# Performance work log

Hardware: AMD Instinct MI355X
Metric: run time of the kernel (lower is better)

## Reference

```python
import jax, jax.numpy as jnp
import numpy as np

N_SENT = 20  # sentence_number


def setup_inputs() -> dict:
    key = jax.random.key(0)
    k1, k2, k3, k4, k5 = jax.random.split(key, 5)
    B, S, D, U = 2048, 800, 100, 50
    inputs = jax.random.normal(k1, (B, S + 1, D), dtype=jnp.float32)
    # keras 'random_normal' initializer default stddev = 0.05
    vw = 0.05 * jax.random.normal(k2, (U, 1), dtype=jnp.float32)
    wh = 0.05 * jax.random.normal(k3, (U, D), dtype=jnp.float32)
    wu = 0.05 * jax.random.normal(k4, (U, D), dtype=jnp.float32)
    bw = 0.05 * jax.random.normal(k5, (U, 1), dtype=jnp.float32)
    return {"inputs": inputs, "vw": vw, "wh": wh, "wu": wu, "bw": bw}


def reference(inputs, vw, wh, wu, bw):
    # inputs: [B, S+1, D]; last row of each item is the user vector
    sent = inputs[:, :-1, :]          # [B, S, D]
    uvec = inputs[:, -1, :]           # [B, D]
    B, S, D = sent.shape
    sec = S // N_SENT
    h = sent.reshape(B, N_SENT, sec, D)               # sections of sentences
    # wu @ user_vec + bw  -> per-batch additive bias  [B, units]
    wub = uvec @ wu.T + bw[:, 0]
    # tanh(h @ wh.T + wub)                              [B, n, s, units]
    t = jnp.tanh(jnp.einsum('bnsd,ud->bnsu', h, wh) + wub[:, None, None, :])
    e = jnp.einsum('bnsu,u->bns', t, vw[:, 0])          # attention logits
    alpha = jax.nn.softmax(e, axis=-1)                  # softmax over section
    out = jnp.einsum('bns,bnsd->bnd', alpha, h)         # weighted pooling
    return out  # [B, N_SENT, D]
```

## Files before the change

kernel.cpp:

```cpp
#include <hip/hip_runtime.h>
#include <hip/hip_bf16.h>
#include <stdint.h>

#define NB    2048
#define NSENT 20
#define SEC   40
#define DD    100
#define UU    50
#define SP1   801
#define STRIDE 136

typedef short bf16x8 __attribute__((ext_vector_type(8)));
typedef float f32x4 __attribute__((ext_vector_type(4)));

__device__ __forceinline__ unsigned f2bf(float f) {
  unsigned u = __float_as_uint(f);
  return (u + 0x7fffu + ((u >> 16) & 1u)) >> 16;
}

__global__ __launch_bounds__(256, 4) void doc_kernel(
    const float* __restrict__ inputs, const float* __restrict__ vw,
    const float* __restrict__ wh, const float* __restrict__ wu,
    const float* __restrict__ bw, float* __restrict__ out) {
  __shared__ __align__(16) unsigned short hs[2][48 * STRIDE];
  __shared__ __align__(16) float epart[3 * 16 * 4];

  const int tid  = threadIdx.x;
  const int w    = tid >> 6, lane = tid & 63;
  const int col  = lane & 15, grp = lane >> 4;
  const int b    = blockIdx.x;

  const float4* base4 = (const float4*)(inputs + (size_t)b * SP1 * DD);

  float4 stA[4], stB[4];
  #pragma unroll
  for (int j = 0; j < 4; ++j) stA[j] = base4[j * 256 + tid];
  #pragma unroll
  for (int j = 0; j < 4; ++j) stB[j] = base4[1000 + j * 256 + tid];

  {
    uint4 z; z.x = z.y = z.z = z.w = 0u;
    uint4* p = (uint4*)&hs[0][0];
    #pragma unroll 1
    for (int i = tid; i < 2 * 48 * STRIDE / 8; i += 256) p[i] = z;
  }

  int cvta[4];
  #pragma unroll
  for (int j = 0; j < 4; ++j) {
    int idx = j * 256 + tid;
    int row = idx / 25, c4 = idx - row * 25;
    cvta[j] = row * 272 + c4 * 8;
  }

  bf16x8 afrag[4];
  {
    int u = w * 16 + col;
    #pragma unroll
    for (int kt = 0; kt < 4; ++kt) {
      bf16x8 f;
      #pragma unroll
      for (int j = 0; j < 8; ++j) {
        int k = kt * 32 + grp * 8 + j;
        float v = (u < UU && k < DD) ? wh[u * DD + k] : 0.f;
        f[j] = (short)f2bf(v);
      }
      afrag[kt] = f;
    }
  }

  float wubacc;
  {
    int ur = lane < UU ? lane : UU - 1;
    const float4* uv4 = (const float4*)(inputs + ((size_t)b * SP1 + SP1 - 1) * DD);
    const float4* wr4 = (const float4*)(wu + ur * DD);
    float a0 = bw[ur];
    #pragma unroll 5
    for (int q = 0; q < 25; ++q) {
      float4 uq = uv4[q], wq = wr4[q];
      a0 = fmaf(uq.x, wq.x, a0); a0 = fmaf(uq.y, wq.y, a0);
      a0 = fmaf(uq.z, wq.z, a0); a0 = fmaf(uq.w, wq.w, a0);
    }
    wubacc = a0;
  }
  float vwr[4], wubr[4];
  #pragma unroll
  for (int r = 0; r < 4; ++r) {
    int u = w * 16 + grp * 4 + r;
    float wv = __shfl(wubacc, u & 63);
    bool val = (u < UU);
    vwr[r]  = val ? vw[u] : 0.f;
    wubr[r] = val ? wv : 0.f;
  }

  __syncthreads();

  float* outb = out + (size_t)b * NSENT * DD;

#define TILE_BODY(stg, t)                                                      \
  {                                                                            \
    unsigned char* hc = (unsigned char*)&hs[(t) & 1][0];                       \
                     \
    _Pragma("unroll")                                                          \
    for (int j = 0; j < 4; ++j) {                                              \
      unsigned o0, o1;                                                         \
      asm("v_cvt_pk_bf16_f32 %0, %1, %2" : "=v"(o0) : "v"(stg[j].x), "v"(stg[j].y)); \
      asm("v_cvt_pk_bf16_f32 %0, %1, %2" : "=v"(o1) : "v"(stg[j].z), "v"(stg[j].w)); \
      uint2 wv; wv.x = o0; wv.y = o1;                                          \
      *(uint2*)(hc + cvta[j]) = wv;                                            \
    }                                                                          \
      \
    if ((t) + 2 < NSENT) {                                                     \
      const float4* nb4 = base4 + (size_t)((t) + 2) * 1000;                    \
      _Pragma("unroll")                                                        \
      for (int j = 0; j < 4; ++j) stg[j] = nb4[j * 256 + tid];                 \
    }                                                                          \
    __builtin_amdgcn_sched_barrier(0);                                         \
    __syncthreads();                                                   \
                                   \
    f32x4 acc[3];                                                              \
    _Pragma("unroll")                                                          \
    for (int st = 0; st < 3; ++st) { f32x4 z = {0.f,0.f,0.f,0.f}; acc[st] = z; } \
    _Pragma("unroll")                                                          \
    for (int kt = 0; kt < 4; ++kt) {                                           \
      _Pragma("unroll")                                                        \
      for (int st = 0; st < 3; ++st) {                                         \
        bf16x8 hf = *(const bf16x8*)(hc + (st * 16 + col) * 272 + kt * 64 + grp * 16); \
        acc[st] = __builtin_amdgcn_mfma_f32_16x16x32_bf16(afrag[kt], hf, acc[st], 0, 0, 0); \
      }                                                                        \
    }                                                                          \
                                \
    _Pragma("unroll")                                                          \
    for (int st = 0; st < 3; ++st) {                                           \
      float s = 0.f;                                                           \
      _Pragma("unroll")                                                        \
      for (int r = 0; r < 4; ++r) {                                            \
        float x = acc[st][r] + wubr[r];                                        \
        float E = __expf(2.f * x);                                             \
        float tt = 1.f - 2.f * __builtin_amdgcn_rcpf(E + 1.f);                 \
        s = fmaf(tt, vwr[r], s);                                               \
      }                                                                        \
      s += __shfl_xor(s, 16);                                                  \
      s += __shfl_xor(s, 32);                                                  \
      if (grp == 0) epart[st * 64 + col * 4 + w] = s;                          \
    }                                                                          \
    __syncthreads();                                                   \
             \
    int sl = lane < SEC ? lane : 0;                                            \
    f32x4 q = *(const f32x4*)&epart[(sl >> 4) * 64 + (sl & 15) * 4];           \
    float e = (q[0] + q[1]) + (q[2] + q[3]);                                   \
    float p = (lane < SEC) ? __expf(e) : 0.f;                                  \
    float sum = p;                                                             \
    sum += __shfl_xor(sum, 1);                                                 \
    sum += __shfl_xor(sum, 2);                                                 \
    sum += __shfl_xor(sum, 4);                                                 \
    sum += __shfl_xor(sum, 8);                                                 \
    sum += __shfl_xor(sum, 16);                                                \
    sum += __shfl_xor(sum, 32);                                                \
    float pr = p * __builtin_amdgcn_rcpf(sum);                                 \
        \
    asm volatile("" : "+v"(pr));                                               \
                  \
    if (lane < 25) {                                                           \
      int d = 25 * w + lane;                                                   \
      const unsigned short* hp = (const unsigned short*)hc + d;                \
      float a0 = 0.f, a1 = 0.f;                                                \
      _Pragma("unroll")                                                        \
      for (int s = 0; s < SEC; s += 2) {                                       \
        float al0 = __uint_as_float(__builtin_amdgcn_readlane(__float_as_uint(pr), s));     \
        float al1 = __uint_as_float(__builtin_amdgcn_readlane(__float_as_uint(pr), s + 1)); \
        a0 = fmaf(al0, __uint_as_float((unsigned)hp[s * STRIDE] << 16), a0);   \
        a1 = fmaf(al1, __uint_as_float((unsigned)hp[(s + 1) * STRIDE] << 16), a1); \
      }                                                                        \
      outb[(t) * DD + d] = a0 + a1;                                            \
    }                                                                          \
  }

  #pragma unroll 1
  for (int t = 0; t < NSENT; t += 2) {
    TILE_BODY(stA, t)
    TILE_BODY(stB, t + 1)
  }
#undef TILE_BODY
}

extern "C" void kernel_launch(void* const* d_in, const int* in_sizes, int n_in,
                              void* d_out, int out_size, void* d_ws, size_t ws_size,
                              hipStream_t stream) {
  const float* inputs = (const float*)d_in[0];
  const float* vw     = (const float*)d_in[1];
  const float* wh     = (const float*)d_in[2];
  const float* wu     = (const float*)d_in[3];
  const float* bw     = (const float*)d_in[4];
  float* out = (float*)d_out;

  doc_kernel<<<NB, 256, 0, stream>>>(inputs, vw, wh, wu, bw, out);
}
```

Before: 162.0 us.

## Process two sentence sections per tile to halve barrier iterations

Each tile now covers two 40-row sections (80 rows), so the loop runs ten iterations instead of twenty. The staging registers double to eight float4s per buffer, and MFMA work per tile rises to five 16-row sub-tiles. Pooling is split so each pair of waves handles one section and half of the D dimension. The aim is to cut per-tile synchronisation and softmax overhead and to keep more loads in flight. In exchange, register and LDS use grow and launch bounds drop to three blocks per CU, which lowers occupancy.

```diff
diff --git a/kernel.cpp b/kernel.cpp
--- a/kernel.cpp
+++ b/kernel.cpp
@@ -9,6 +9,9 @@
 #define UU    50
 #define SP1   801
 #define STRIDE 136
+#define TROWS 80
+#define TGRAN 2000
+#define MAXG  20024
 
 typedef short bf16x8 __attribute__((ext_vector_type(8)));
 typedef float f32x4 __attribute__((ext_vector_type(4)));
@@ -18,12 +21,12 @@
   return (u + 0x7fffu + ((u >> 16) & 1u)) >> 16;
 }
 
-__global__ __launch_bounds__(256, 4) void doc_kernel(
+__global__ __launch_bounds__(256, 3) void doc_kernel(
     const float* __restrict__ inputs, const float* __restrict__ vw,
     const float* __restrict__ wh, const float* __restrict__ wu,
     const float* __restrict__ bw, float* __restrict__ out) {
-  __shared__ __align__(16) unsigned short hs[2][48 * STRIDE];
-  __shared__ __align__(16) float epart[3 * 16 * 4];
+  __shared__ __align__(16) unsigned short hs[2][TROWS * STRIDE];
+  __shared__ __align__(16) float epart[5 * 16 * 4];
 
   const int tid  = threadIdx.x;
   const int w    = tid >> 6, lane = tid & 63;
@@ -32,22 +35,22 @@
 
   const float4* base4 = (const float4*)(inputs + (size_t)b * SP1 * DD);
 
-  float4 stA[4], stB[4];
-  #pragma unroll
-  for (int j = 0; j < 4; ++j) stA[j] = base4[j * 256 + tid];
-  #pragma unroll
-  for (int j = 0; j < 4; ++j) stB[j] = base4[1000 + j * 256 + tid];
+  float4 stA[8], stB[8];
+  #pragma unroll
+  for (int j = 0; j < 8; ++j) stA[j] = base4[min(j * 256 + tid, MAXG)];
+  #pragma unroll
+  for (int j = 0; j < 8; ++j) stB[j] = base4[min(TGRAN + j * 256 + tid, MAXG)];
 
   {
     uint4 z; z.x = z.y = z.z = z.w = 0u;
     uint4* p = (uint4*)&hs[0][0];
     #pragma unroll 1
-    for (int i = tid; i < 2 * 48 * STRIDE / 8; i += 256) p[i] = z;
-  }
-
-  int cvta[4];
-  #pragma unroll
-  for (int j = 0; j < 4; ++j) {
+    for (int i = tid; i < 2 * TROWS * STRIDE / 8; i += 256) p[i] = z;
+  }
+
+  int cvta[8];
+  #pragma unroll
+  for (int j = 0; j < 8; ++j) {
     int idx = j * 256 + tid;
     int row = idx / 25, c4 = idx - row * 25;
     cvta[j] = row * 272 + c4 * 8;
@@ -96,42 +99,46 @@
   __syncthreads();
 
   float* outb = out + (size_t)b * NSENT * DD;
+  const int sent = w >> 1, dh = w & 1;
 
 #define TILE_BODY(stg, t)                                                      \
   {                                                                            \
     unsigned char* hc = (unsigned char*)&hs[(t) & 1][0];                       \
                      \
     _Pragma("unroll")                                                          \
-    for (int j = 0; j < 4; ++j) {                                              \
-      unsigned o0, o1;                                                         \
-      asm("v_cvt_pk_bf16_f32 %0, %1, %2" : "=v"(o0) : "v"(stg[j].x), "v"(stg[j].y)); \
-      asm("v_cvt_pk_bf16_f32 %0, %1, %2" : "=v"(o1) : "v"(stg[j].z), "v"(stg[j].w)); \
-      uint2 wv; wv.x = o0; wv.y = o1;                                          \
-      *(uint2*)(hc + cvta[j]) = wv;                                            \
-    }                                                                          \
-      \
-    if ((t) + 2 < NSENT) {                                                     \
-      const float4* nb4 = base4 + (size_t)((t) + 2) * 1000;                    \
-      _Pragma("unroll")                                                        \
-      for (int j = 0; j < 4; ++j) stg[j] = nb4[j * 256 + tid];                 \
+    for (int j = 0; j < 8; ++j) {                                              \
+      int idx = j * 256 + tid;                                                 \
+      if (j < 7 || idx < TGRAN) {                                              \
+        unsigned o0, o1;                                                       \
+        asm("v_cvt_pk_bf16_f32 %0, %1, %2" : "=v"(o0) : "v"(stg[j].x), "v"(stg[j].y)); \
+        asm("v_cvt_pk_bf16_f32 %0, %1, %2" : "=v"(o1) : "v"(stg[j].z), "v"(stg[j].w)); \
+        uint2 wv; wv.x = o0; wv.y = o1;                                        \
+        *(uint2*)(hc + cvta[j]) = wv;                                          \
+      }                                                                        \
+    }                                                                          \
+                           \
+    if ((t) + 2 < NSENT / 2) {                                                 \
+      _Pragma("unroll")                                                        \
+      for (int j = 0; j < 8; ++j)                                              \
+        stg[j] = base4[min(((t) + 2) * TGRAN + j * 256 + tid, MAXG)];          \
     }                                                                          \
     __builtin_amdgcn_sched_barrier(0);                                         \
     __syncthreads();                                                   \
-                                   \
-    f32x4 acc[3];                                                              \
-    _Pragma("unroll")                                                          \
-    for (int st = 0; st < 3; ++st) { f32x4 z = {0.f,0.f,0.f,0.f}; acc[st] = z; } \
+                          \
+    f32x4 acc[5];                                                              \
+    _Pragma("unroll")                                                          \
+    for (int st = 0; st < 5; ++st) { f32x4 z = {0.f,0.f,0.f,0.f}; acc[st] = z; } \
     _Pragma("unroll")                                                          \
     for (int kt = 0; kt < 4; ++kt) {                                           \
       _Pragma("unroll")                                                        \
-      for (int st = 0; st < 3; ++st) {                                         \
+      for (int st = 0; st < 5; ++st) {                                         \
         bf16x8 hf = *(const bf16x8*)(hc + (st * 16 + col) * 272 + kt * 64 + grp * 16); \
         acc[st] = __builtin_amdgcn_mfma_f32_16x16x32_bf16(afrag[kt], hf, acc[st], 0, 0, 0); \
       }                                                                        \
     }                                                                          \
                                 \
     _Pragma("unroll")                                                          \
-    for (int st = 0; st < 3; ++st) {                                           \
+    for (int st = 0; st < 5; ++st) {                                           \
       float s = 0.f;                                                           \
       _Pragma("unroll")                                                        \
       for (int r = 0; r < 4; ++r) {                                            \
@@ -145,9 +152,9 @@
       if (grp == 0) epart[st * 64 + col * 4 + w] = s;                          \
     }                                                                          \
     __syncthreads();                                                   \
-             \
-    int sl = lane < SEC ? lane : 0;                                            \
-    f32x4 q = *(const f32x4*)&epart[(sl >> 4) * 64 + (sl & 15) * 4];           \
+          \
+    int srow = sent * SEC + (lane < SEC ? lane : 0);                           \
+    f32x4 q = *(const f32x4*)&epart[(srow >> 4) * 64 + (srow & 15) * 4];       \
     float e = (q[0] + q[1]) + (q[2] + q[3]);                                   \
     float p = (lane < SEC) ? __expf(e) : 0.f;                                  \
     float sum = p;                                                             \
@@ -160,10 +167,10 @@
     float pr = p * __builtin_amdgcn_rcpf(sum);                                 \
         \
     asm volatile("" : "+v"(pr));                                               \
-                  \
-    if (lane < 25) {                                                           \
-      int d = 25 * w + lane;                                                   \
-      const unsigned short* hp = (const unsigned short*)hc + d;                \
+     \
+    if (lane < 50) {                                                           \
+      int d = dh * 50 + lane;                                                  \
+      const unsigned short* hp = (const unsigned short*)hc + sent * SEC * STRIDE + d; \
       float a0 = 0.f, a1 = 0.f;                                                \
       _Pragma("unroll")                                                        \
       for (int s = 0; s < SEC; s += 2) {                                       \
@@ -172,12 +179,12 @@
         a0 = fmaf(al0, __uint_as_float((unsigned)hp[s * STRIDE] << 16), a0);   \
         a1 = fmaf(al1, __uint_as_float((unsigned)hp[(s + 1) * STRIDE] << 16), a1); \
       }                                                                        \
-      outb[(t) * DD + d] = a0 + a1;                                            \
+      outb[((t) * 2 + sent) * DD + d] = a0 + a1;                               \
     }                                                                          \
   }
 
   #pragma unroll 1
-  for (int t = 0; t < NSENT; t += 2) {
+  for (int t = 0; t < NSENT / 2; t += 2) {
     TILE_BODY(stA, t)
     TILE_BODY(stB, t + 1)
   }
```

New measurement: 155.3 us. 4.1% less time.
